# Performance work log

Hardware: AMD Instinct MI355X
Metric: run time of the kernel (lower is better)

Reference implementation:

```python
import jax, jax.numpy as jnp
import numpy as np

N, K, M, H, F = 4, 1024, 1024, 16, 4096
D = M // H  # per-head dim (dim_q = dim_v = 64)
EPS = 1e-5


def _mha(q_in, k_in, v_in, Wq, bq, Wk, bk, Wv, bv, Wo, bo, mask):
    # Wq/Wk/Wv: [H, M, D]; bq/bk/bv: [H, D]; Wo: [H*D, M]; bo: [M]
    q = jnp.einsum('nkm,hmd->nhkd', q_in, Wq) + bq[None, :, None, :]
    k = jnp.einsum('nkm,hmd->nhkd', k_in, Wk) + bk[None, :, None, :]
    v = jnp.einsum('nkm,hmd->nhkd', v_in, Wv) + bv[None, :, None, :]
    scores = jnp.einsum('nhkd,nhld->nhkl', q, k) / jnp.sqrt(jnp.asarray(D, q.dtype))
    if mask is not None:
        scores = jnp.where(mask[:, None, :, :] == 0, jnp.asarray(-jnp.inf, q.dtype), scores)
    attn = jax.nn.softmax(scores, axis=-1)          # [N,H,K,K]
    y = jnp.einsum('nhkl,nhld->nhkd', attn, v)      # [N,H,K,D]
    y = y.transpose(0, 2, 1, 3).reshape(q_in.shape[0], q_in.shape[1], -1)  # concat heads -> [N,K,H*D]
    return y @ Wo + bo


def _ln(x, g, b):
    mu = jnp.mean(x, axis=-1, keepdims=True)
    var = jnp.mean((x - mu) ** 2, axis=-1, keepdims=True)
    return (x - mu) * jax.lax.rsqrt(var + EPS) * g + b


def setup_inputs() -> dict:
    key = jax.random.key(0)
    ks = jax.random.split(key, 24)
    s = 0.02
    def rn(k, shape):
        return jax.random.normal(k, shape, dtype=jnp.float32) * s
    inp = {
        'dec_inp': jax.random.normal(ks[0], (N, K, M), dtype=jnp.float32),
        'enc_out': jax.random.normal(ks[1], (N, K, M), dtype=jnp.float32),
        'mask': jnp.tril(jnp.ones((K, K), dtype=jnp.int32))[None].repeat(N, axis=0),
        # self-attention params
        'Wq_s': rn(ks[2], (H, M, D)), 'bq_s': jnp.zeros((H, D)),
        'Wk_s': rn(ks[3], (H, M, D)), 'bk_s': jnp.zeros((H, D)),
        'Wv_s': rn(ks[4], (H, M, D)), 'bv_s': jnp.zeros((H, D)),
        'Wo_s': rn(ks[5], (H * D, M)), 'bo_s': jnp.zeros((M,)),
        # cross-attention params
        'Wq_c': rn(ks[6], (H, M, D)), 'bq_c': jnp.zeros((H, D)),
        'Wk_c': rn(ks[7], (H, M, D)), 'bk_c': jnp.zeros((H, D)),
        'Wv_c': rn(ks[8], (H, M, D)), 'bv_c': jnp.zeros((H, D)),
        'Wo_c': rn(ks[9], (H * D, M)), 'bo_c': jnp.zeros((M,)),
        # feedforward params
        'W1': rn(ks[10], (M, F)), 'b1': jnp.zeros((F,)),
        'W2': rn(ks[11], (F, M)), 'b2': jnp.zeros((M,)),
        # layernorm params
        'g1': jnp.ones((M,)), 'be1': jnp.zeros((M,)),
        'g2': jnp.ones((M,)), 'be2': jnp.zeros((M,)),
        'g3': jnp.ones((M,)), 'be3': jnp.zeros((M,)),
    }
    return inp


def reference(dec_inp, enc_out, mask,
              Wq_s, bq_s, Wk_s, bk_s, Wv_s, bv_s, Wo_s, bo_s,
              Wq_c, bq_c, Wk_c, bk_c, Wv_c, bv_c, Wo_c, bo_c,
              W1, b1, W2, b2, g1, be1, g2, be2, g3, be3):
    # masked self-attention + residual + LN (dropout = identity in eval)
    out1 = _mha(dec_inp, dec_inp, dec_inp, Wq_s, bq_s, Wk_s, bk_s, Wv_s, bv_s, Wo_s, bo_s, mask)
    out2 = _ln(dec_inp + out1, g1, be1)
    # cross-attention with encoder output + residual + LN
    out3 = _mha(out2, enc_out, enc_out, Wq_c, bq_c, Wk_c, bk_c, Wv_c, bv_c, Wo_c, bo_c, None)
    out4 = _ln(out3 + out2, g2, be2)
    # feedforward + residual + LN
    out5 = jax.nn.relu(out4 @ W1 + b1) @ W2 + b2
    return _ln(out5 + out4, g3, be3)
```

## Files before the change

### kernel.cpp

```cpp
#include <hip/hip_runtime.h>

#define NB   4
#define SEQ  1024
#define MD   1024
#define NH   16
#define HD   64
#define FF   4096
#define NK   (NB*SEQ)
#define EPSF 1e-5f
#define QS   3072

typedef short short8 __attribute__((ext_vector_type(8)));
typedef float f32x4  __attribute__((ext_vector_type(4)));
typedef unsigned short u16;
typedef unsigned int u32;

__device__ __forceinline__ u16 f2bf(float x) {
    union { float f; unsigned u; } v; v.f = x;
    unsigned r = v.u + 0x7FFF + ((v.u >> 16) & 1);
    return (u16)(r >> 16);
}
__device__ __forceinline__ u16 f2bf_trunc(float x) {
    union { float f; unsigned u; } v; v.f = x;
    return (u16)(v.u >> 16);
}
__device__ __forceinline__ float bf2f(u16 x) {
    union { unsigned u; float f; } v; v.u = ((unsigned)x) << 16;
    return v.f;
}
__device__ __forceinline__ void gload_lds16(const void* g, void* l) {
    __builtin_amdgcn_global_load_lds(
        (const __attribute__((address_space(1))) unsigned int*)g,
        (__attribute__((address_space(3))) unsigned int*)l,
        16, 0, 0);
}

__global__ __launch_bounds__(256) void conv_bf16(const float* __restrict__ s0,
                                                 const float* __restrict__ s1,
                                                 u16* __restrict__ d0,
                                                 u16* __restrict__ d1) {
    const float* S = blockIdx.y ? s1 : s0;
    u16* D = blockIdx.y ? d1 : d0;
    const int i = blockIdx.x * 256 + threadIdx.x;
    float4 v = ((const float4*)S)[i];
    ushort4 o;
    o.x = f2bf(v.x); o.y = f2bf(v.y); o.z = f2bf(v.z); o.w = f2bf(v.w);
    ((ushort4*)D)[i] = o;
}

__global__ __launch_bounds__(256) void mask_tiles(const int* __restrict__ mask,
                                                  int* __restrict__ cls,
                                                  u32* __restrict__ bits) {
    const int jt = blockIdx.x, qt = blockIdx.y, n = blockIdx.z;
    const int t = threadIdx.x;
    const int r = t >> 1, h2 = (t & 1) * 2;
    u32 bb[2];
#pragma unroll
    for (int sg = 0; sg < 2; ++sg) {
        const int* mp = &mask[((size_t)n * SEQ + qt * 128 + r) * SEQ + jt * 128 + (h2 + sg) * 32];
        u32 b = 0;
#pragma unroll
        for (int k = 0; k < 8; ++k) {
            int4 v = *(const int4*)(mp + k * 4);
            b |= (v.x ? 1u : 0u) << (k * 4 + 0);
            b |= (v.y ? 1u : 0u) << (k * 4 + 1);
            b |= (v.z ? 1u : 0u) << (k * 4 + 2);
            b |= (v.w ? 1u : 0u) << (k * 4 + 3);
        }
        bb[sg] = b;
    }
    const int tile = (n * 8 + qt) * 8 + jt;
    bits[((size_t)tile * 128 + r) * 4 + h2]     = bb[0];
    bits[((size_t)tile * 128 + r) * 4 + h2 + 1] = bb[1];
    const int nfull  = __syncthreads_count(bb[0] == 0xFFFFFFFFu && bb[1] == 0xFFFFFFFFu);
    const int nempty = __syncthreads_count(bb[0] == 0u && bb[1] == 0u);
    if (t == 0) cls[tile] = (nfull == 256) ? 2 : ((nempty == 256) ? 0 : 1);
}

struct QkvArgs { const float* src[6]; u16* dst[6]; };

__global__ __launch_bounds__(256) void repack_qkv(QkvArgs a) {
    const int m0 = blockIdx.x * 64;
    const int h  = blockIdx.y;
    const int w  = blockIdx.z;
    const float* W = a.src[w];
    u16* BT = a.dst[w];
    const int t = threadIdx.x;
    __shared__ u16 Ts[64][72];

    const int r = t >> 4, c4 = (t & 15) * 4;
#pragma unroll
    for (int p = 0; p < 4; ++p) {
        const int row = r + p * 16;
        float4 v = *(const float4*)&W[((size_t)h * 1024 + m0 + row) * 64 + c4];
        Ts[row][c4] = f2bf(v.x); Ts[row][c4 + 1] = f2bf(v.y);
        Ts[row][c4 + 2] = f2bf(v.z); Ts[row][c4 + 3] = f2bf(v.w);
    }
    __syncthreads();
    const int d = t >> 2, j0 = (t & 3) * 16;
#pragma unroll
    for (int p = 0; p < 4; ++p) {
        ushort4 o;
        o.x = Ts[j0 + p * 4 + 0][d]; o.y = Ts[j0 + p * 4 + 1][d];
        o.z = Ts[j0 + p * 4 + 2][d]; o.w = Ts[j0 + p * 4 + 3][d];
        *(ushort4*)&BT[((size_t)h * 64 + d) * 1024 + m0 + j0 + p * 4] = o;
    }
}

struct FD { const float* src; int ss; u16* dst; int ds; };
struct FlatArgs { FD d[10]; };

__global__ __launch_bounds__(256) void repack_flat(FlatArgs fa) {
    FD u = fa.d[blockIdx.z];
    const int r0 = blockIdx.x * 64;
    const int c0 = blockIdx.y * 64;
    const int t  = threadIdx.x;
    __shared__ u16 Ts[64][72];

    const int r = t >> 4, c4 = (t & 15) * 4;
#pragma unroll
    for (int p = 0; p < 4; ++p) {
        const int row = r + p * 16;
        float4 v = *(const float4*)&u.src[(size_t)(r0 + row) * u.ss + c0 + c4];
        Ts[row][c4] = f2bf(v.x); Ts[row][c4 + 1] = f2bf(v.y);
        Ts[row][c4 + 2] = f2bf(v.z); Ts[row][c4 + 3] = f2bf(v.w);
    }
    __syncthreads();
    const int d = t >> 2, j0 = (t & 3) * 16;
#pragma unroll
    for (int p = 0; p < 4; ++p) {
        ushort4 o;
        o.x = Ts[j0 + p * 4 + 0][d]; o.y = Ts[j0 + p * 4 + 1][d];
        o.z = Ts[j0 + p * 4 + 2][d]; o.w = Ts[j0 + p * 4 + 3][d];
        *(ushort4*)&u.dst[(size_t)(c0 + d) * u.ds + r0 + j0 + p * 4] = o;
    }
}

template<int OUT_BF16, int RELU, int RESID, int BIAS3, int PARTIAL, int VT>
__global__ __launch_bounds__(256) void gemm_mfma(const u16* __restrict__ A,
                                                 const u16* __restrict__ A2,
                                                 int Astride,
                                                 const u16* __restrict__ BT,
                                                 int Bstride,
                                                 const float* __restrict__ b0,
                                                 const float* __restrict__ b1p,
                                                 const float* __restrict__ b2p,
                                                 const float* __restrict__ resid,
                                                 void* __restrict__ Cout,
                                                 u16* __restrict__ VtOut,
                                                 int Kd, int Nd) {
    const int nt = blockIdx.x;
    const int mt = blockIdx.y;
    const int t  = threadIdx.x;
    const int wave = t >> 6, lane = t & 63;
    const int q = lane >> 4, l16 = lane & 15;
    const int wm = wave >> 1, wn = wave & 1;

    __shared__ __align__(16) u16 As[128 * 64];
    __shared__ __align__(16) u16 Bs[128 * 64];

    const int row0 = mt * 128, col0 = nt * 128;
    const u16* Ause = (col0 < 1024) ? A : A2;
    const int kBase = PARTIAL ? blockIdx.z * Kd : 0;

    f32x4 acc[4][4];
#pragma unroll
    for (int r = 0; r < 4; ++r)
#pragma unroll
        for (int c = 0; c < 4; ++c) acc[r][c] = (f32x4)0.0f;

    const int lrow = lane >> 3;
    const int lcb  = lane & 7;

    for (int k0 = 0; k0 < Kd; k0 += 64) {
        __syncthreads();
#pragma unroll
        for (int p = 0; p < 4; ++p) {
            const int rr = wave * 32 + p * 8 + lrow;
            const int gcb = lcb ^ (rr & 7);
            gload_lds16(Ause + (size_t)(row0 + rr) * Astride + kBase + k0 + gcb * 8, As + (size_t)(wave * 32 + p * 8) * 64);
            gload_lds16(BT   + (size_t)(col0 + rr) * Bstride + kBase + k0 + gcb * 8, Bs + (size_t)(wave * 32 + p * 8) * 64);
        }
        __syncthreads();

#pragma unroll
        for (int s = 0; s < 2; ++s) {
            const int pb = (q + s * 4) ^ (l16 & 7);
            short8 af[4], bf[4];
#pragma unroll
            for (int r = 0; r < 4; ++r)
                af[r] = *(const short8*)&As[(wm * 64 + r * 16 + l16) * 64 + pb * 8];
#pragma unroll
            for (int c = 0; c < 4; ++c)
                bf[c] = *(const short8*)&Bs[(wn * 64 + c * 16 + l16) * 64 + pb * 8];
#pragma unroll
            for (int r = 0; r < 4; ++r)
#pragma unroll
                for (int c = 0; c < 4; ++c)
                    acc[r][c] = __builtin_amdgcn_mfma_f32_16x16x32_bf16(af[r], bf[c], acc[r][c], 0, 0, 0);
        }
    }

    float* Pout = PARTIAL ? ((float*)Cout + (size_t)blockIdx.z * NK * Nd) : nullptr;

#pragma unroll
    for (int c = 0; c < 4; ++c) {
        const int col = col0 + wn * 64 + c * 16 + l16;
        float bb = 0.0f;
        if (!PARTIAL) {
            if (BIAS3) {
                const int sec = col >> 10;
                const float* bp = sec == 0 ? b0 : (sec == 1 ? b1p : b2p);
                bb = bp[col & 1023];
            } else {
                bb = b0[col];
            }
        }
#pragma unroll
        for (int r = 0; r < 4; ++r) {
#pragma unroll
            for (int reg = 0; reg < 4; ++reg) {
                const int row = row0 + wm * 64 + r * 16 + q * 4 + reg;
                float v = acc[r][c][reg] + bb;
                if (PARTIAL) {
                    Pout[(size_t)row * Nd + col] = acc[r][c][reg];
                } else {
                    if (RELU)  v = fmaxf(v, 0.0f);
                    if (RESID) v += resid[(size_t)row * Nd + col];
                    if (OUT_BF16) ((u16*)Cout)[(size_t)row * Nd + col] = f2bf(v);
                    else          ((float*)Cout)[(size_t)row * Nd + col] = v;
                }
            }
        }
    }
}

template<int OUT_BF16, int RELU, int BIAS3, int PARTIAL, int VT>
__global__ __launch_bounds__(512, 2) void gemm256p(const u16* __restrict__ A,
                                                   const u16* __restrict__ A2,
                                                   int Astride,
                                                   const u16* __restrict__ BT,
                                                   int Bstride,
                                                   const float* __restrict__ b0,
                                                   const float* __restrict__ b1p,
                                                   const float* __restrict__ b2p,
                                                   void* __restrict__ Cout,
                                                   u16* __restrict__ VtOut,
                                                   int Kd, int Nd, int swzW) {
    const int t  = threadIdx.x;
    const int wave = t >> 6, lane = t & 63;
    const int q = lane >> 4, l16 = lane & 15;
    const int wm = wave >> 1, wn = wave & 1;
    const int x7 = l16 & 7;

    const int gx = gridDim.x;
    const int bid = blockIdx.x + blockIdx.y * gx;
    const int cpx = (gx * gridDim.y) >> 3;
    const int xcd = bid & 7;
    const int cc  = bid >> 3;
    const int regNX = gx / swzW;
    const int mtspan = cpx / swzW;
    const int nt = (xcd % regNX) * swzW + cc % swzW;
    const int mt = (xcd / regNX) * mtspan + cc / swzW;

    extern __shared__ __align__(16) char smem[];
    u16* As = (u16*)smem;
    u16* Bs = (u16*)(smem + 3 * 256 * 64 * 2);

    const int row0 = mt * 256, col0 = nt * 128;
    const u16* Ause = (col0 < 1024) ? A : A2;
    const int kBase = PARTIAL ? blockIdx.z * Kd : 0;

    f32x4 acc[4][4];
#pragma unroll
    for (int r = 0; r < 4; ++r)
#pragma unroll
        for (int c = 0; c < 4; ++c) acc[r][c] = (f32x4)0.0f;

    const int lrow = lane >> 3;
    const int lcb  = lane & 7;

    auto stagePart = [&](int slot, int kk, int part) {
#pragma unroll
        for (int p = 0; p < 2; ++p) {
            const int rr = wave * 32 + (part * 2 + p) * 8 + lrow;
            const int gcb = lcb ^ (rr & 7);
            gload_lds16(Ause + (size_t)(row0 + rr) * Astride + kk + gcb * 8,
                        As + slot * (256 * 64) + (wave * 32 + (part * 2 + p) * 8) * 64);
        }
        {
            const int rr = wave * 16 + part * 8 + lrow;
            const int gcb = lcb ^ (rr & 7);
            gload_lds16(BT + (size_t)(col0 + rr) * Bstride + kk + gcb * 8,
                        Bs + slot * (128 * 64) + (wave * 16 + part * 8) * 64);
        }
    };

    const int nsteps = Kd / 64;
    stagePart(0, kBase, 0);      stagePart(0, kBase, 1);
    stagePart(1, kBase + 64, 0); stagePart(1, kBase + 64, 1);

    int st = 0, st2 = 2;
    for (int it = 0; it < nsteps; ++it) {
        const int kk2 = kBase + (it + 2) * 64;
        const u16* Ab = As + st * (256 * 64);
        const u16* Bb = Bs + st * (128 * 64);

        if (it + 2 < nsteps) {
            stagePart(st2, kk2, 0);
            asm volatile("s_waitcnt vmcnt(9)" ::: "memory");
        } else if (it + 1 < nsteps) {
            asm volatile("s_waitcnt vmcnt(6)" ::: "memory");
        } else {
            asm volatile("s_waitcnt vmcnt(0)" ::: "memory");
        }
        __builtin_amdgcn_s_barrier();
        {
            const int pb = q ^ x7;
            short8 af[4], bf[4];
#pragma unroll
            for (int r = 0; r < 4; ++r)
                af[r] = *(const short8*)&Ab[(wm * 64 + r * 16 + l16) * 64 + pb * 8];
#pragma unroll
            for (int c = 0; c < 4; ++c)
                bf[c] = *(const short8*)&Bb[(wn * 64 + c * 16 + l16) * 64 + pb * 8];
            __builtin_amdgcn_s_setprio(1);
#pragma unroll
            for (int r = 0; r < 4; ++r)
#pragma unroll
                for (int c = 0; c < 4; ++c)
                    acc[r][c] = __builtin_amdgcn_mfma_f32_16x16x32_bf16(af[r], bf[c], acc[r][c], 0, 0, 0);
            __builtin_amdgcn_s_setprio(0);
        }
        __builtin_amdgcn_s_barrier();

        if (it + 2 < nsteps) stagePart(st2, kk2, 1);
        {
            const int pb = (q + 4) ^ x7;
            short8 af[4], bf[4];
#pragma unroll
            for (int r = 0; r < 4; ++r)
                af[r] = *(const short8*)&Ab[(wm * 64 + r * 16 + l16) * 64 + pb * 8];
#pragma unroll
            for (int c = 0; c < 4; ++c)
                bf[c] = *(const short8*)&Bb[(wn * 64 + c * 16 + l16) * 64 + pb * 8];
            __builtin_amdgcn_s_barrier();
            asm volatile("s_waitcnt lgkmcnt(0)" ::: "memory");
            __builtin_amdgcn_sched_barrier(0);
            __builtin_amdgcn_s_setprio(1);
#pragma unroll
            for (int r = 0; r < 4; ++r)
#pragma unroll
                for (int c = 0; c < 4; ++c)
                    acc[r][c] = __builtin_amdgcn_mfma_f32_16x16x32_bf16(af[r], bf[c], acc[r][c], 0, 0, 0);
            __builtin_amdgcn_s_setprio(0);
        }
        __builtin_amdgcn_s_barrier();

        st  = (st  == 2) ? 0 : st + 1;
        st2 = (st2 == 2) ? 0 : st2 + 1;
    }

    if (VT && col0 >= 2048) {
#pragma unroll
        for (int c = 0; c < 4; ++c) {
            const int col = col0 + wn * 64 + c * 16 + l16;
            const float bb = b2p[col & 1023];
            const int d = col & 63, hh = (col >> 6) & 15;
#pragma unroll
            for (int r = 0; r < 4; ++r) {
                const int row = row0 + wm * 64 + r * 16 + q * 4;
                const int nn = row >> 10, k = row & 1023;
                ushort4 o;
                o.x = f2bf(acc[r][c][0] + bb);
                o.y = f2bf(acc[r][c][1] + bb);
                o.z = f2bf(acc[r][c][2] + bb);
                o.w = f2bf(acc[r][c][3] + bb);
                *(ushort4*)&VtOut[((size_t)(nn * 16 + hh) * 64 + d) * 1024 + k] = o;
            }
        }
        return;
    }

    float* Pout = PARTIAL ? ((float*)Cout + (size_t)blockIdx.z * NK * Nd) : nullptr;

#pragma unroll
    for (int c = 0; c < 4; ++c) {
        const int col = col0 + wn * 64 + c * 16 + l16;
        float bb = 0.0f;
        if (!PARTIAL) {
            if (BIAS3) {
                const int sec = col >> 10;
                const float* bp = sec == 0 ? b0 : (sec == 1 ? b1p : b2p);
                bb = bp[col & 1023];
            } else {
                bb = b0[col];
            }
        }
#pragma unroll
        for (int r = 0; r < 4; ++r) {
#pragma unroll
            for (int reg = 0; reg < 4; ++reg) {
                const int row = row0 + wm * 64 + r * 16 + q * 4 + reg;
                float v = acc[r][c][reg] + bb;
                if (PARTIAL) {
                    Pout[(size_t)row * Nd + col] = acc[r][c][reg];
                } else {
                    if (RELU)  v = fmaxf(v, 0.0f);
                    if (OUT_BF16) ((u16*)Cout)[(size_t)row * Nd + col] = f2bf(v);
                    else          ((float*)Cout)[(size_t)row * Nd + col] = v;
                }
            }
        }
    }
}

#define PSTR 136
#define ATTN_LDS (128*64*2 + 64*128*2 + 8*16*PSTR*2)

__global__ __launch_bounds__(512, 4) void attn_mfma(const u16* __restrict__ QKV,
                                                    const u16* __restrict__ Vt,
                                                    const int* __restrict__ cls,
                                                    const u32* __restrict__ bits,
                                                    u16* __restrict__ Yout) {
    const int qt = blockIdx.x;
    const int h  = blockIdx.y;
    const int n  = blockIdx.z;
    const int t  = threadIdx.x;
    const int wave = t >> 6;
    const int lane = t & 63;
    const int quad = lane >> 4;
    const int l16  = lane & 15;
    const int sw   = wave >> 2;
    const int wq   = wave & 3;

    extern __shared__ __align__(16) char smem[];
    u16* Ks = (u16*)smem;
    u16* Vs = (u16*)(smem + 128 * 64 * 2);
    u16* Pw = (u16*)(smem + 128 * 64 * 2 + 64 * 128 * 2) + wave * 16 * PSTR;

    const int bh = n * NH + h;
    const int i0 = qt * 128;

    int cl[8];
    if (cls) {
        const int* cp = &cls[(n * 8 + qt) * 8];
#pragma unroll
        for (int j = 0; j < 8; ++j) cl[j] = cp[j];
    } else {
#pragma unroll
        for (int j = 0; j < 8; ++j) cl[j] = 2;
    }

    short8 qf[2];
    {
        const u16* qrow = QKV + ((size_t)n * SEQ + i0 + sw * 64 + wq * 16 + l16) * QS + h * 64 + quad * 8;
        short8 a = *(const short8*)(qrow);
        short8 b = *(const short8*)(qrow + 32);
#pragma unroll
        for (int j = 0; j < 8; ++j) {
            qf[0][j] = (short)f2bf(bf2f((u16)a[j]) * 0.18033688f);
            qf[1][j] = (short)f2bf(bf2f((u16)b[j]) * 0.18033688f);
        }
    }

    f32x4 O[4];
#pragma unroll
    for (int d = 0; d < 4; ++d) O[d] = (f32x4)0.0f;
    float lrow[4] = {};

    const int krow = lane >> 3, kblk = lane & 7;
    const int vrow = lane >> 4, vblk = lane & 15;
    const int x7 = l16 & 7;

    for (int jt = 0; jt < SEQ / 128; ++jt) {
        const int c = cl[jt];
        if (c == 0) continue;
        __syncthreads();

#pragma unroll
        for (int p = 0; p < 2; ++p) {
            const int rr = wave * 16 + p * 8 + krow;
            const int kb = kblk ^ (rr & 7);
            gload_lds16(QKV + ((size_t)n * SEQ + jt * 128 + rr) * QS + 1024 + h * 64 + kb * 8,
                        Ks + (wave * 16 + p * 8) * 64);
        }
#pragma unroll
        for (int p = 0; p < 2; ++p) {
            const int rr = wave * 8 + p * 4 + vrow;
            const int kb = vblk ^ (rr & 15);
            gload_lds16(Vt + ((size_t)bh * HD + rr) * SEQ + jt * 128 + kb * 8,
                        Vs + (wave * 8 + p * 4) * 128);
        }
        __syncthreads();

        f32x4 S[8];
#pragma unroll
        for (int sub = 0; sub < 8; ++sub) {
            S[sub] = (f32x4)0.0f;
            const int row = sub * 16 + l16;
            short8 k0 = *(const short8*)&Ks[row * 64 + ((quad ^ x7) * 8)];
            S[sub] = __builtin_amdgcn_mfma_f32_16x16x32_bf16(qf[0], k0, S[sub], 0, 0, 0);
            short8 k1 = *(const short8*)&Ks[row * 64 + (((4 + quad) ^ x7) * 8)];
            S[sub] = __builtin_amdgcn_mfma_f32_16x16x32_bf16(qf[1], k1, S[sub], 0, 0, 0);
        }

        if (c == 1) {
#pragma unroll
            for (int reg = 0; reg < 4; ++reg) {
                const int row = sw * 64 + wq * 16 + quad * 4 + reg;
                const uint4 mm = *(const uint4*)&bits[((size_t)((n * 8 + qt) * 8 + jt) * 128 + row) * 4];
#pragma unroll
                for (int sub = 0; sub < 8; ++sub) {
                    const u32 seg = (sub >> 1) == 0 ? mm.x : (sub >> 1) == 1 ? mm.y : (sub >> 1) == 2 ? mm.z : mm.w;
                    if (!((seg >> ((sub & 1) * 16 + l16)) & 1u)) S[sub][reg] = -1e30f;
                }
            }
        }

#pragma unroll
        for (int reg = 0; reg < 4; ++reg) {
            float rs = 0.0f;
#pragma unroll
            for (int sub = 0; sub < 8; ++sub) {
                float e = exp2f(S[sub][reg]);
                Pw[(quad * 4 + reg) * PSTR + sub * 16 + l16] = f2bf_trunc(e);
                rs += e;
            }
            rs += __shfl_xor(rs, 1);
            rs += __shfl_xor(rs, 2);
            rs += __shfl_xor(rs, 4);
            rs += __shfl_xor(rs, 8);
            lrow[reg] += rs;
        }

        short8 pa[4];
#pragma unroll
        for (int ks = 0; ks < 4; ++ks)
            pa[ks] = *(const short8*)&Pw[l16 * PSTR + ks * 32 + quad * 8];
#pragma unroll
        for (int d = 0; d < 4; ++d) {
            const int row = d * 16 + l16;
#pragma unroll
            for (int ks = 0; ks < 4; ++ks) {
                short8 vb = *(const short8*)&Vs[row * 128 + (((ks * 4 + quad) ^ l16) & 15) * 8];
                O[d] = __builtin_amdgcn_mfma_f32_16x16x32_bf16(pa[ks], vb, O[d], 0, 0, 0);
            }
        }
    }

#pragma unroll
    for (int d = 0; d < 4; ++d) {
#pragma unroll
        for (int reg = 0; reg < 4; ++reg) {
            const int row = i0 + sw * 64 + wq * 16 + quad * 4 + reg;
            const int col = h * 64 + d * 16 + l16;
            Yout[((size_t)n * SEQ + row) * QS + col] = f2bf(O[d][reg] / lrow[reg]);
        }
    }
}

__global__ __launch_bounds__(256) void ln_kernel(const float* __restrict__ X,
                                                 const float* __restrict__ g,
                                                 const float* __restrict__ be,
                                                 float* __restrict__ Y,
                                                 u16* __restrict__ Yb) {
    const int row = blockIdx.x;
    const int t = threadIdx.x;
    __shared__ float red[256];

    const float4 v = ((const float4*)(X + (size_t)row * MD))[t];
    red[t] = v.x + v.y + v.z + v.w;
    __syncthreads();
    for (int s2 = 128; s2 > 0; s2 >>= 1) {
        if (t < s2) red[t] += red[t + s2];
        __syncthreads();
    }
    const float mu = red[0] * (1.0f / MD);
    __syncthreads();

    float dx = v.x - mu, dy = v.y - mu, dz = v.z - mu, dw = v.w - mu;
    red[t] = dx * dx + dy * dy + dz * dz + dw * dw;
    __syncthreads();
    for (int s2 = 128; s2 > 0; s2 >>= 1) {
        if (t < s2) red[t] += red[t + s2];
        __syncthreads();
    }
    const float var = red[0] * (1.0f / MD);
    const float rs = rsqrtf(var + EPSF);

    const float4 gv = ((const float4*)g)[t];
    const float4 bv = ((const float4*)be)[t];
    float4 o;
    o.x = dx * rs * gv.x + bv.x;
    o.y = dy * rs * gv.y + bv.y;
    o.z = dz * rs * gv.z + bv.z;
    o.w = dw * rs * gv.w + bv.w;
    if (Y) ((float4*)(Y + (size_t)row * MD))[t] = o;
    if (Yb) {
        ushort4 ob;
        ob.x = f2bf(o.x); ob.y = f2bf(o.y); ob.z = f2bf(o.z); ob.w = f2bf(o.w);
        ((ushort4*)(Yb + (size_t)row * MD))[t] = ob;
    }
}

__global__ __launch_bounds__(256) void ln_fused2(const float* __restrict__ p0,
                                                 const float* __restrict__ p1,
                                                 const float* __restrict__ bias,
                                                 const float* __restrict__ resid,
                                                 const float* __restrict__ g,
                                                 const float* __restrict__ be,
                                                 float* __restrict__ Y) {
    const int row = blockIdx.x;
    const int t = threadIdx.x;
    __shared__ float red[256];

    const float4 a = ((const float4*)(p0 + (size_t)row * MD))[t];
    const float4 b = ((const float4*)(p1 + (size_t)row * MD))[t];
    const float4 r = ((const float4*)(resid + (size_t)row * MD))[t];
    const float4 bi = ((const float4*)bias)[t];
    float4 v;
    v.x = a.x + b.x + r.x + bi.x;
    v.y = a.y + b.y + r.y + bi.y;
    v.z = a.z + b.z + r.z + bi.z;
    v.w = a.w + b.w + r.w + bi.w;

    red[t] = v.x + v.y + v.z + v.w;
    __syncthreads();
    for (int s2 = 128; s2 > 0; s2 >>= 1) {
        if (t < s2) red[t] += red[t + s2];
        __syncthreads();
    }
    const float mu = red[0] * (1.0f / MD);
    __syncthreads();

    float dx = v.x - mu, dy = v.y - mu, dz = v.z - mu, dw = v.w - mu;
    red[t] = dx * dx + dy * dy + dz * dz + dw * dw;
    __syncthreads();
    for (int s2 = 128; s2 > 0; s2 >>= 1) {
        if (t < s2) red[t] += red[t + s2];
        __syncthreads();
    }
    const float var = red[0] * (1.0f / MD);
    const float rs = rsqrtf(var + EPSF);

    const float4 gv = ((const float4*)g)[t];
    const float4 bv = ((const float4*)be)[t];
    float4 o;
    o.x = dx * rs * gv.x + bv.x;
    o.y = dy * rs * gv.y + bv.y;
    o.z = dz * rs * gv.z + bv.z;
    o.w = dw * rs * gv.w + bv.w;
    ((float4*)(Y + (size_t)row * MD))[t] = o;
}

extern "C" void kernel_launch(void* const* d_in, const int* in_sizes, int n_in,
                              void* d_out, int out_size, void* d_ws, size_t ws_size,
                              hipStream_t stream) {
    const float* dec  = (const float*)d_in[0];
    const float* enc  = (const float*)d_in[1];
    const int*   mask = (const int*)d_in[2];
    const float* Wq_s = (const float*)d_in[3];
    const float* bq_s = (const float*)d_in[4];
    const float* Wk_s = (const float*)d_in[5];
    const float* bk_s = (const float*)d_in[6];
    const float* Wv_s = (const float*)d_in[7];
    const float* bv_s = (const float*)d_in[8];
    const float* Wo_s = (const float*)d_in[9];
    const float* bo_s = (const float*)d_in[10];
    const float* Wq_c = (const float*)d_in[11];
    const float* bq_c = (const float*)d_in[12];
    const float* Wk_c = (const float*)d_in[13];
    const float* bk_c = (const float*)d_in[14];
    const float* Wv_c = (const float*)d_in[15];
    const float* bv_c = (const float*)d_in[16];
    const float* Wo_c = (const float*)d_in[17];
    const float* bo_c = (const float*)d_in[18];
    const float* W1   = (const float*)d_in[19];
    const float* b1   = (const float*)d_in[20];
    const float* W2   = (const float*)d_in[21];
    const float* b2   = (const float*)d_in[22];
    const float* g1   = (const float*)d_in[23];
    const float* be1  = (const float*)d_in[24];
    const float* g2   = (const float*)d_in[25];
    const float* be2  = (const float*)d_in[26];
    const float* g3   = (const float*)d_in[27];
    const float* be3  = (const float*)d_in[28];

    char* wsb = (char*)d_ws;
    const size_t MB = 1u << 20;
    u16*   decb  = (u16*)(wsb + 0 * MB);
    u16*   O2b   = (u16*)(wsb + 0 * MB);
    u16*   encb  = (u16*)(wsb + 8 * MB);
    u16*   O4b   = (u16*)(wsb + 8 * MB);
    u16*   WqkvsT= (u16*)(wsb + 16 * MB);
    u16*   WqkvcT= (u16*)(wsb + 22 * MB);
    u16*   WosT  = (u16*)(wsb + 28 * MB);
    u16*   WocT  = (u16*)(wsb + 30 * MB);
    u16*   W1T   = (u16*)(wsb + 32 * MB);
    u16*   W2T   = (u16*)(wsb + 40 * MB);
    u16*   QKVb  = (u16*)(wsb + 48 * MB);
    u16*   Vt    = (u16*)(wsb + 72 * MB);
    u16*   Hb    = (u16*)(wsb + 48 * MB);
    int*   mcls  = (int*)(wsb + 80 * MB);
    u32*   mbits = (u32*)(wsb + 80 * MB + 64 * 1024);
    float* Tb    = (float*)(wsb + 80 * MB);
    float* FP    = (float*)(wsb + 0 * MB);
    float* O2    = (float*)(wsb + 96 * MB);
    float* O4    = (float*)(wsb + 96 * MB);

    dim3 blk(256);
    dim3 blkA(512);
    dim3 blkG(512);
    dim3 gConv(NK * MD / 4 / 256, 2);
    dim3 gMask(8, 8, 4);
    dim3 gQkvW(16, 16, 6);
    dim3 gFlatW(16, 16, 10);
    dim3 gAttn(SEQ / 128, NH, NB);
    dim3 gQKV(QS / 128, NK / 256);
    dim3 gOut(MD / 128, NK / 128);
    dim3 gF1(FF / 128, NK / 256);
    dim3 gF2(MD / 128, NK / 256, 2);
    const int GP_LDS = 3 * (256 * 64 + 128 * 64) * 2;

    conv_bf16<<<gConv, blk, 0, stream>>>(dec, enc, decb, encb);
    mask_tiles<<<gMask, blk, 0, stream>>>(mask, mcls, mbits);

    QkvArgs qa;
    qa.src[0] = Wq_s; qa.src[1] = Wk_s; qa.src[2] = Wv_s;
    qa.src[3] = Wq_c; qa.src[4] = Wk_c; qa.src[5] = Wv_c;
    qa.dst[0] = WqkvsT;                 qa.dst[1] = WqkvsT + (size_t)1024 * 1024;
    qa.dst[2] = WqkvsT + (size_t)2048 * 1024;
    qa.dst[3] = WqkvcT;                 qa.dst[4] = WqkvcT + (size_t)1024 * 1024;
    qa.dst[5] = WqkvcT + (size_t)2048 * 1024;
    repack_qkv<<<gQkvW, blk, 0, stream>>>(qa);

    FlatArgs fa;
    fa.d[0] = { Wo_s, 1024, WosT, 1024 };
    fa.d[1] = { Wo_c, 1024, WocT, 1024 };
    for (int u = 0; u < 4; ++u)
        fa.d[2 + u] = { W1 + (size_t)u * 1024, 4096, W1T + (size_t)u * 1024 * 1024, 1024 };
    for (int u = 0; u < 4; ++u)
        fa.d[6 + u] = { W2 + (size_t)u * 1024 * 1024, 1024, W2T + (size_t)u * 1024, 4096 };
    repack_flat<<<gFlatW, blk, 0, stream>>>(fa);

    gemm256p<1, 0, 1, 0, 1><<<gQKV, blkG, GP_LDS, stream>>>(decb, decb, MD, WqkvsT, MD, bq_s, bk_s, bv_s, QKVb, Vt, MD, QS, 6);
    attn_mfma<<<gAttn, blkA, ATTN_LDS, stream>>>(QKVb, Vt, mcls, mbits, QKVb);
    gemm_mfma<0, 0, 1, 0, 0, 0><<<gOut, blk, 0, stream>>>(QKVb, QKVb, QS, WosT, MD, bo_s, nullptr, nullptr, dec, Tb, nullptr, MD, MD);
    ln_kernel<<<NK, blk, 0, stream>>>(Tb, g1, be1, O2, O2b);

    gemm256p<1, 0, 1, 0, 1><<<gQKV, blkG, GP_LDS, stream>>>(O2b, encb, MD, WqkvcT, MD, bq_c, bk_c, bv_c, QKVb, Vt, MD, QS, 6);
    attn_mfma<<<gAttn, blkA, ATTN_LDS, stream>>>(QKVb, Vt, nullptr, nullptr, QKVb);
    gemm_mfma<0, 0, 1, 0, 0, 0><<<gOut, blk, 0, stream>>>(QKVb, QKVb, QS, WocT, MD, bo_c, nullptr, nullptr, O2, Tb, nullptr, MD, MD);
    ln_kernel<<<NK, blk, 0, stream>>>(Tb, g2, be2, O4, O4b);

    gemm256p<1, 1, 0, 0, 0><<<gF1, blkG, GP_LDS, stream>>>(O4b, O4b, MD, W1T, MD, b1, nullptr, nullptr, Hb, nullptr, MD, FF, 8);
    gemm256p<0, 0, 0, 1, 0><<<gF2, blkG, GP_LDS, stream>>>(Hb, Hb, FF, W2T, FF, nullptr, nullptr, nullptr, FP, nullptr, FF / 2, MD, 2);
    ln_fused2<<<NK, blk, 0, stream>>>(FP, FP + (size_t)NK * MD, b2, O4, g3, be3, (float*)d_out);
}
```

Baseline: 362.7 us.

## Restructure GEMM k-loop to load both LDS halves upfront and use one barrier

Rewrites the main GEMM k-step loop to wait once for the current stage, read both k-halves of the A/B fragments from LDS up front, then issue the prefetch and both MFMA blocks without further barriers. This removes three of the four workgroup barriers per k-step and the explicit lgkmcnt/sched_barrier fencing. The triple-buffered staging is meant to keep the reuse safe, and the cost is more live fragment registers, which may reduce occupancy.

After: 342.0 us. 1.06x faster.

```diff
diff --git a/kernel.cpp b/kernel.cpp
--- a/kernel.cpp
+++ b/kernel.cpp
@@ -302,60 +302,48 @@
 
     int st = 0, st2 = 2;
     for (int it = 0; it < nsteps; ++it) {
-        const int kk2 = kBase + (it + 2) * 64;
+        if (it + 1 < nsteps) asm volatile("s_waitcnt vmcnt(6)" ::: "memory");
+        else                 asm volatile("s_waitcnt vmcnt(0)" ::: "memory");
+        __builtin_amdgcn_s_barrier();
+
         const u16* Ab = As + st * (256 * 64);
         const u16* Bb = Bs + st * (128 * 64);
-
-        if (it + 2 < nsteps) {
-            stagePart(st2, kk2, 0);
-            asm volatile("s_waitcnt vmcnt(9)" ::: "memory");
-        } else if (it + 1 < nsteps) {
-            asm volatile("s_waitcnt vmcnt(6)" ::: "memory");
-        } else {
-            asm volatile("s_waitcnt vmcnt(0)" ::: "memory");
-        }
-        __builtin_amdgcn_s_barrier();
-        {
-            const int pb = q ^ x7;
-            short8 af[4], bf[4];
-#pragma unroll
-            for (int r = 0; r < 4; ++r)
-                af[r] = *(const short8*)&Ab[(wm * 64 + r * 16 + l16) * 64 + pb * 8];
+        const int pb0 = q ^ x7;
+        const int pb1 = (q + 4) ^ x7;
+
+        short8 af0[4], bf0[4], af1[4], bf1[4];
+#pragma unroll
+        for (int r = 0; r < 4; ++r) {
+            af0[r] = *(const short8*)&Ab[(wm * 64 + r * 16 + l16) * 64 + pb0 * 8];
+            af1[r] = *(const short8*)&Ab[(wm * 64 + r * 16 + l16) * 64 + pb1 * 8];
+        }
+#pragma unroll
+        for (int c = 0; c < 4; ++c) {
+            bf0[c] = *(const short8*)&Bb[(wn * 64 + c * 16 + l16) * 64 + pb0 * 8];
+            bf1[c] = *(const short8*)&Bb[(wn * 64 + c * 16 + l16) * 64 + pb1 * 8];
+        }
+
+        const bool pre = (it + 2 < nsteps);
+        const int kk2 = kBase + (it + 2) * 64;
+        if (pre) stagePart(st2, kk2, 0);
+
+        __builtin_amdgcn_s_setprio(1);
+#pragma unroll
+        for (int r = 0; r < 4; ++r)
 #pragma unroll
             for (int c = 0; c < 4; ++c)
-                bf[c] = *(const short8*)&Bb[(wn * 64 + c * 16 + l16) * 64 + pb * 8];
-            __builtin_amdgcn_s_setprio(1);
-#pragma unroll
-            for (int r = 0; r < 4; ++r)
-#pragma unroll
-                for (int c = 0; c < 4; ++c)
-                    acc[r][c] = __builtin_amdgcn_mfma_f32_16x16x32_bf16(af[r], bf[c], acc[r][c], 0, 0, 0);
-            __builtin_amdgcn_s_setprio(0);
-        }
-        __builtin_amdgcn_s_barrier();
-
-        if (it + 2 < nsteps) stagePart(st2, kk2, 1);
-        {
-            const int pb = (q + 4) ^ x7;
-            short8 af[4], bf[4];
-#pragma unroll
-            for (int r = 0; r < 4; ++r)
-                af[r] = *(const short8*)&Ab[(wm * 64 + r * 16 + l16) * 64 + pb * 8];
+                acc[r][c] = __builtin_amdgcn_mfma_f32_16x16x32_bf16(af0[r], bf0[c], acc[r][c], 0, 0, 0);
+        __builtin_amdgcn_s_setprio(0);
+
+        if (pre) stagePart(st2, kk2, 1);
+
+        __builtin_amdgcn_s_setprio(1);
+#pragma unroll
+        for (int r = 0; r < 4; ++r)
 #pragma unroll
             for (int c = 0; c < 4; ++c)
-                bf[c] = *(const short8*)&Bb[(wn * 64 + c * 16 + l16) * 64 + pb * 8];
-            __builtin_amdgcn_s_barrier();
-            asm volatile("s_waitcnt lgkmcnt(0)" ::: "memory");
-            __builtin_amdgcn_sched_barrier(0);
-            __builtin_amdgcn_s_setprio(1);
-#pragma unroll
-            for (int r = 0; r < 4; ++r)
-#pragma unroll
-                for (int c = 0; c < 4; ++c)
-                    acc[r][c] = __builtin_amdgcn_mfma_f32_16x16x32_bf16(af[r], bf[c], acc[r][c], 0, 0, 0);
-            __builtin_amdgcn_s_setprio(0);
-        }
-        __builtin_amdgcn_s_barrier();
+                acc[r][c] = __builtin_amdgcn_mfma_f32_16x16x32_bf16(af1[r], bf1[c], acc[r][c], 0, 0, 0);
+        __builtin_amdgcn_s_setprio(0);
 
         st  = (st  == 2) ? 0 : st + 1;
         st2 = (st2 == 2) ? 0 : st2 + 1;
```
